# Kernel optimization log

Hardware: AMD Instinct MI355X
Metric: run time of the kernel (lower is better)

## Reference

```python
import jax, jax.numpy as jnp
import numpy as np
import math

NO, NR, E = 100000, 1000, 1000000
DO, DR, DE, H, OM = 64, 32, 4, 64, 32


def setup_inputs() -> dict:
    key = jax.random.key(0)
    ks = jax.random.split(key, 20)
    s = lambda k, sh: jax.random.normal(k, sh, dtype=jnp.float32) * 0.05
    inp = {
        'x_order': jax.random.normal(ks[0], (NO, DO), dtype=jnp.float32),
        'x_rider': jax.random.normal(ks[1], (NR, DR), dtype=jnp.float32),
        'edge_attr': jax.random.normal(ks[2], (E, DE), dtype=jnp.float32),
        'order_idx': jax.random.randint(ks[3], (E,), 0, NO),
        'rider_idx': jax.random.randint(ks[4], (E,), 0, NR),
        'omega_encoded': jax.random.normal(ks[5], (OM,), dtype=jnp.float32),
        # TransformerConv params (heads=1)
        'Wk': s(ks[6], (DO, H)), 'bk': jnp.zeros((H,), jnp.float32),
        'Wq': s(ks[7], (DR, H)), 'bq': jnp.zeros((H,), jnp.float32),
        'Wv': s(ks[8], (DO, H)), 'bv': jnp.zeros((H,), jnp.float32),
        'We': s(ks[9], (DE, H)),  # lin_edge, bias=False in PyG
        'Wskip': s(ks[10], (DR, H)), 'bskip': jnp.zeros((H,), jnp.float32),
        # order_proj
        'Wp': s(ks[11], (DO, H)), 'bp': jnp.zeros((H,), jnp.float32),
        # residual MLP: Linear(2H+OM,128) -> ReLU -> Linear(128,1)
        'W1': s(ks[12], (2 * H + OM, 128)), 'b1': jnp.zeros((128,), jnp.float32),
        'W2': s(ks[13], (128, 1)), 'b2': jnp.zeros((1,), jnp.float32),
    }
    return inp


def _segment_softmax(alpha, seg, num_segments):
    m = jax.ops.segment_max(alpha, seg, num_segments=num_segments)
    m = jnp.where(jnp.isfinite(m), m, 0.0)
    ex = jnp.exp(alpha - m[seg])
    denom = jax.ops.segment_sum(ex, seg, num_segments=num_segments)
    return ex / (denom[seg] + 1e-16)


def reference(x_order, x_rider, edge_attr, order_idx, rider_idx, omega_encoded,
              Wk, bk, Wq, bq, Wv, bv, We, Wskip, bskip, Wp, bp, W1, b1, W2, b2):
    scale = 1.0 / math.sqrt(H)
    # TransformerConv((order, rider) -> rider), heads=1, edge_dim
    q = x_rider @ Wq + bq            # [NR, H]
    k = x_order @ Wk + bk            # [NO, H]
    v = x_order @ Wv + bv            # [NO, H]
    e = edge_attr @ We               # [E, H]
    k_j = k[order_idx] + e           # [E, H]
    v_j = v[order_idx] + e           # [E, H]
    alpha = jnp.sum(q[rider_idx] * k_j, axis=-1) * scale  # [E]
    alpha = _segment_softmax(alpha, rider_idx, NR)
    agg = jax.ops.segment_sum(alpha[:, None] * v_j, rider_idx, num_segments=NR)  # [NR, H]
    rider_emb = agg + x_rider @ Wskip + bskip  # root/skip connection

    # edge scoring
    order_proj = x_order @ Wp + bp   # [NO, H]
    oe = order_proj[order_idx]       # [E, H]
    re = rider_emb[rider_idx]        # [E, H]
    dot = jnp.sum(oe * re, axis=-1) * scale  # [E]
    omega_expand = jnp.broadcast_to(omega_encoded[None, :], (oe.shape[0], OM))
    resid_in = jnp.concatenate([oe, re, omega_expand], axis=-1)  # [E, 2H+OM]
    hmid = jax.nn.relu(resid_in @ W1 + b1)
    resid = (hmid @ W2 + b2)[:, 0]
    return jnp.clip(dot + resid, -10.0, 10.0)
```

## Files before the change

### kernel.cpp

```cpp
#include <hip/hip_runtime.h>
#include <hip/hip_bf16.h>
#include <math.h>
#include <stdint.h>

#define NO_N 100000
#define NR_N 1000
#define E_N  1000000
#define SB     250
#define SCHUNK 4000
#define KVP_TILES 1563
#define KVP_BLKS 1024
#define MAXTILES 17008

typedef short bf16x8 __attribute__((ext_vector_type(8)));
typedef float floatx4 __attribute__((ext_vector_type(4)));

__device__ __forceinline__ unsigned short bfu(float x) {
    union { __hip_bfloat16 h; unsigned short u; } c;
    c.h = __float2bfloat16(x);
    return c.u;
}
__device__ __forceinline__ float bflo(unsigned int u) {
    return __uint_as_float(u << 16);
}
__device__ __forceinline__ float bfhi(unsigned int u) {
    return __uint_as_float(u & 0xffff0000u);
}

__global__ __launch_bounds__(256) void k_front(
    const float* __restrict__ xr,
    const float* __restrict__ Wq, const float* __restrict__ bq,
    const float* __restrict__ Wskip, const float* __restrict__ bskip,
    const float* __restrict__ We,
    float* __restrict__ q, float* __restrict__ skip, float* __restrict__ t,
    const float* __restrict__ W1, const float* __restrict__ b1,
    const float* __restrict__ omega, float* __restrict__ b1eff,
    unsigned short* __restrict__ w1t,
    const float* __restrict__ x,
    const float* __restrict__ Wk, const float* __restrict__ bk,
    const float* __restrict__ Wv, const float* __restrict__ bv,
    const float* __restrict__ Wp, const float* __restrict__ bp,
    unsigned short* __restrict__ kb, unsigned short* __restrict__ vb,
    unsigned short* __restrict__ pb,
    const int* __restrict__ ridx, int* __restrict__ ghist)
{
    __shared__ __align__(16) char smem[9216];
    const int tid = threadIdx.x;
    const int b = blockIdx.x;

    if (b < 250) {
        float* sx = (float*)smem;
        float* sq = sx + 128;
        int rbase = b * 4;
        if (tid < 128) {
            int rl = tid >> 5, d = tid & 31;
            sx[rl * 32 + d] = xr[(rbase + rl) * 32 + d];
        }
        __syncthreads();
        int rl = tid >> 6, h = tid & 63;
        int r = rbase + rl;
        float aq = bq[h], as = bskip[h];
        #pragma unroll 4
        for (int d = 0; d < 32; ++d) {
            float xv = sx[rl * 32 + d];
            aq += xv * Wq[d * 64 + h];
            as += xv * Wskip[d * 64 + h];
        }
        sq[rl * 64 + h] = aq;
        q[r * 64 + h] = aq;
        skip[r * 64 + h] = as;
        __syncthreads();
        if (tid < 16) {
            int rl2 = tid >> 2, d = tid & 3;
            float acc = 0.f;
            for (int hh = 0; hh < 64; ++hh)
                acc += We[d * 64 + hh] * sq[rl2 * 64 + hh];
            t[(rbase + rl2) * 4 + d] = acc;
        }
    } else if (b == 250) {
        if (tid < 128) {
            float acc = b1[tid];
            #pragma unroll 4
            for (int j = 0; j < 32; ++j)
                acc += omega[j] * W1[(128 + j) * 128 + tid];
            b1eff[tid] = acc;
        }
        for (int idx = tid; idx < 64 * 128; idx += 256) {
            int n = idx >> 6, k = idx & 63;
            w1t[idx] = bfu(W1[k * 128 + n]);
        }
    } else if (b < 251 + KVP_BLKS) {
        unsigned short* sX = (unsigned short*)smem;
        const int wave = tid >> 6, lane = tid & 63;
        const int l15 = lane & 15, quad = lane >> 4;

        bf16x8 bfr[3][2];
        float bias[3];
        unsigned short* outT[3];
        int colc[3];
        #pragma unroll
        for (int ct = 0; ct < 3; ++ct) {
            int n = wave * 48 + ct * 16 + l15;
            int table = n >> 6, c = n & 63;
            const float* W  = (table == 0) ? Wk : (table == 1) ? Wv : Wp;
            const float* bb = (table == 0) ? bk : (table == 1) ? bv : bp;
            bias[ct] = bb[c];
            colc[ct] = c;
            outT[ct] = (table == 0) ? kb : (table == 1) ? vb : pb;
            #pragma unroll
            for (int kf = 0; kf < 2; ++kf) {
                bf16x8 f;
                #pragma unroll
                for (int j = 0; j < 8; ++j)
                    f[j] = (short)bfu(W[(size_t)(kf * 32 + quad * 8 + j) * 64 + c]);
                bfr[ct][kf] = f;
            }
        }

        const int srl = tid >> 2;
        const int sqt = (tid & 3) * 16;

        for (int tile = b - 251; tile < KVP_TILES; tile += KVP_BLKS) {
            int rowbase = tile * 64;
            {
                int row = rowbase + srl;
                unsigned short* dst = sX + srl * 72 + sqt;
                if (row < NO_N) {
                    const float4* src = (const float4*)(x + (size_t)row * 64 + sqt);
                    #pragma unroll
                    for (int i = 0; i < 4; ++i) {
                        float4 a = src[i];
                        ushort4 u = { bfu(a.x), bfu(a.y), bfu(a.z), bfu(a.w) };
                        *(ushort4*)(dst + i * 4) = u;
                    }
                } else {
                    ushort4 z = {0, 0, 0, 0};
                    #pragma unroll
                    for (int i = 0; i < 4; ++i) *(ushort4*)(dst + i * 4) = z;
                }
            }
            __syncthreads();

            floatx4 acc[4][3];
            #pragma unroll
            for (int rt = 0; rt < 4; ++rt)
                #pragma unroll
                for (int ct = 0; ct < 3; ++ct)
                    acc[rt][ct] = (floatx4){bias[ct], bias[ct], bias[ct], bias[ct]};

            #pragma unroll
            for (int rt = 0; rt < 4; ++rt) {
                const unsigned short* ar = sX + (size_t)(rt * 16 + l15) * 72 + quad * 8;
                bf16x8 a0 = *(const bf16x8*)(ar);
                bf16x8 a1 = *(const bf16x8*)(ar + 32);
                #pragma unroll
                for (int ct = 0; ct < 3; ++ct) {
                    floatx4 c = acc[rt][ct];
                    c = __builtin_amdgcn_mfma_f32_16x16x32_bf16(a0, bfr[ct][0], c, 0, 0, 0);
                    c = __builtin_amdgcn_mfma_f32_16x16x32_bf16(a1, bfr[ct][1], c, 0, 0, 0);
                    acc[rt][ct] = c;
                }
            }

            #pragma unroll
            for (int rt = 0; rt < 4; ++rt) {
                int rb = rowbase + rt * 16 + quad * 4;
                #pragma unroll
                for (int ct = 0; ct < 3; ++ct) {
                    unsigned short* o = outT[ct];
                    size_t cbase = colc[ct];
                    #pragma unroll
                    for (int g = 0; g < 4; ++g) {
                        int row = rb + g;
                        if (row < NO_N)
                            o[(size_t)row * 64 + cbase] = bfu(acc[rt][ct][g]);
                    }
                }
            }
            __syncthreads();
        }
    } else {
        int* hc = (int*)smem;
        int hb = b - (251 + KVP_BLKS);
        for (int i = tid; i < NR_N; i += 256) hc[i] = 0;
        __syncthreads();
        int s = hb * SCHUNK;
        for (int i = s + tid; i < s + SCHUNK; i += 256)
            atomicAdd(&hc[ridx[i]], 1);
        __syncthreads();
        for (int i = tid; i < NR_N; i += 256)
            ghist[i * SB + hb] = hc[i];
    }
}

__global__ __launch_bounds__(256) void k_colscan(const int* __restrict__ ghist,
                                                 int* __restrict__ gpre,
                                                 int* __restrict__ counts)
{
    __shared__ int s[256];
    int tid = threadIdx.x, r = blockIdx.x;
    int v = (tid < SB) ? ghist[r * SB + tid] : 0;
    s[tid] = v;
    __syncthreads();
    for (int off = 1; off < 256; off <<= 1) {
        int tv = (tid >= off) ? s[tid - off] : 0;
        __syncthreads();
        s[tid] += tv;
        __syncthreads();
    }
    if (tid < SB) gpre[r * SB + tid] = s[tid] - v;
    if (tid == 255) counts[r] = s[255];
}

__global__ __launch_bounds__(1024) void k_scan(const int* __restrict__ counts,
                                               int* __restrict__ offsets,
                                               int* __restrict__ tilestart)
{
    __shared__ int s[1024];
    int tid = threadIdx.x;
    int c = (tid < NR_N) ? counts[tid] : 0;
    s[tid] = c;
    __syncthreads();
    for (int off = 1; off < 1024; off <<= 1) {
        int tv = (tid >= off) ? s[tid - off] : 0;
        __syncthreads();
        s[tid] += tv;
        __syncthreads();
    }
    if (tid < NR_N) offsets[tid] = s[tid] - c;
    if (tid == NR_N - 1) offsets[NR_N] = s[tid];
    __syncthreads();
    int tc = (tid < NR_N) ? ((c + 63) >> 6) : 0;
    s[tid] = tc;
    __syncthreads();
    for (int off = 1; off < 1024; off <<= 1) {
        int tv = (tid >= off) ? s[tid - off] : 0;
        __syncthreads();
        s[tid] += tv;
        __syncthreads();
    }
    if (tid < NR_N) tilestart[tid] = s[tid] - tc;
    if (tid == NR_N - 1) tilestart[NR_N] = s[tid];
}

__global__ __launch_bounds__(256) void k_trec(const int* __restrict__ tilestart,
                                              const int* __restrict__ offsets,
                                              int4* __restrict__ trec)
{
    int nt = tilestart[NR_N];
    int t = blockIdx.x * 256 + threadIdx.x;
    if (t >= nt) return;
    int lo = 0, hi = NR_N - 1;
    while (lo < hi) {
        int mid = (lo + hi + 1) >> 1;
        if (tilestart[mid] <= t) lo = mid; else hi = mid - 1;
    }
    trec[t] = make_int4(lo, offsets[lo] + ((t - tilestart[lo]) << 6),
                        offsets[lo + 1], 0);
}

__global__ __launch_bounds__(1024) void k_scatter2(
    const int* __restrict__ ridx, const int* __restrict__ oidx,
    const float* __restrict__ ea, const float* __restrict__ t,
    const int* __restrict__ offsets, const int* __restrict__ gpre,
    const int* __restrict__ ghist,
    int4* __restrict__ spack, int* __restrict__ so, int* __restrict__ rank)
{
    __shared__ int stmp[1024];
    __shared__ int lpre[NR_N];
    __shared__ int lcur[NR_N];
    __shared__ int gbase[NR_N];
    __shared__ __align__(16) int4 sbuf[SCHUNK];
    __shared__ int spos[SCHUNK];

    const int tid = threadIdx.x, b = blockIdx.x;

    int v = (tid < NR_N) ? ghist[tid * SB + b] : 0;
    stmp[tid] = v;
    __syncthreads();
    for (int off = 1; off < 1024; off <<= 1) {
        int tv = (tid >= off) ? stmp[tid - off] : 0;
        __syncthreads();
        stmp[tid] += tv;
        __syncthreads();
    }
    if (tid < NR_N) {
        lpre[tid] = stmp[tid] - v;
        lcur[tid] = 0;
        gbase[tid] = offsets[tid] + gpre[tid * SB + b];
    }
    __syncthreads();

    int s = b * SCHUNK;
    for (int i = s + tid; i < s + SCHUNK; i += 1024) {
        int r = ridx[i];
        int o = oidx[i];
        float4 e4 = *(const float4*)(ea + (size_t)i * 4);
        float4 t4 = *(const float4*)(t + r * 4);
        float h = e4.x * t4.x + e4.y * t4.y + e4.z * t4.z + e4.w * t4.w;
        int old = atomicAdd(&lcur[r], 1);
        int lpos = lpre[r] + old;
        int gp = gbase[r] + old;
        int4 pk;
        pk.x = o;
        pk.y = __float_as_int(h);
        pk.z = (int)((unsigned)bfu(e4.x) | ((unsigned)bfu(e4.y) << 16));
        pk.w = (int)((unsigned)bfu(e4.z) | ((unsigned)bfu(e4.w) << 16));
        sbuf[lpos] = pk;
        spos[lpos] = gp;
        rank[i] = gp;
    }
    __syncthreads();

    for (int l = tid; l < SCHUNK; l += 1024) {
        int4 pk = sbuf[l];
        int gp = spos[l];
        spack[gp] = pk;
        so[gp] = pk.x;
    }
}

__global__ __launch_bounds__(512) void k_rider(
    const int* __restrict__ offsets, const int4* __restrict__ spack,
    const float* __restrict__ q,
    const unsigned short* __restrict__ kb, const unsigned short* __restrict__ vb,
    const float* __restrict__ We, const float* __restrict__ skip,
    const float* __restrict__ W1, const float* __restrict__ b1eff,
    unsigned short* __restrict__ embb, float* __restrict__ Br)
{
    __shared__ float sQ[64];
    __shared__ int2 sOX[8][64];
    __shared__ float rv[8][64];
    __shared__ float re4[8][4];
    __shared__ float rd[8];

    int r = blockIdx.x;
    int wave = threadIdx.x >> 6, lane = threadIdx.x & 63;
    if (threadIdx.x < 64) sQ[threadIdx.x] = q[r * 64 + threadIdx.x];
    __syncthreads();

    int beg = offsets[r], end = offsets[r + 1];
    int cnt = end - beg;
    int chunk = (cnt + 7) >> 3;
    int s0 = beg + wave * chunk;
    int s1 = min(s0 + chunk, end);

    float av0 = 0.f, av1 = 0.f, av2 = 0.f, av3 = 0.f;
    float dsum = 0.f;
    float ag0 = 0.f, ag1 = 0.f, ag2 = 0.f, ag3 = 0.f;
    const float2* sQ2 = (const float2*)sQ;

    for (int jb = s0; jb < s1; jb += 64) {
        int j = jb + lane;
        bool valid = (j < s1);
        int4 pk = make_int4(0, 0, 0, 0);
        if (valid) pk = spack[j];
        int oo = pk.x;
        float h = __int_as_float(pk.y);

        const uint4* krow = (const uint4*)(kb + (size_t)oo * 64);
        uint4 K0 = krow[0], K1 = krow[1], K2 = krow[2], K3 = krow[3];
        uint4 K4 = krow[4], K5 = krow[5], K6 = krow[6], K7 = krow[7];
        float a0 = h, a1 = 0.f, a2 = 0.f, a3 = 0.f;
        #define DOT8(Kv, base, A) { \
            float2 qa = sQ2[(base) + 0]; \
            A = fmaf(bflo(Kv.x), qa.x, A); A = fmaf(bfhi(Kv.x), qa.y, A); \
            float2 qb = sQ2[(base) + 1]; \
            A = fmaf(bflo(Kv.y), qb.x, A); A = fmaf(bfhi(Kv.y), qb.y, A); \
            float2 qc = sQ2[(base) + 2]; \
            A = fmaf(bflo(Kv.z), qc.x, A); A = fmaf(bfhi(Kv.z), qc.y, A); \
            float2 qd = sQ2[(base) + 3]; \
            A = fmaf(bflo(Kv.w), qd.x, A); A = fmaf(bfhi(Kv.w), qd.y, A); }
        DOT8(K0, 0, a0) DOT8(K1, 4, a1) DOT8(K2, 8, a2) DOT8(K3, 12, a3)
        DOT8(K4, 16, a0) DOT8(K5, 20, a1) DOT8(K6, 24, a2) DOT8(K7, 28, a3)
        #undef DOT8
        float acc = (a0 + a1) + (a2 + a3);

        float exv = valid ? __expf(acc * 0.125f) : 0.f;
        dsum += exv;
        unsigned int ez = (unsigned int)pk.z, ew = (unsigned int)pk.w;
        ag0 = fmaf(exv, bflo(ez), ag0);
        ag1 = fmaf(exv, bfhi(ez), ag1);
        ag2 = fmaf(exv, bflo(ew), ag2);
        ag3 = fmaf(exv, bfhi(ew), ag3);

        sOX[wave][lane] = make_int2(oo, __float_as_int(exv));

        int nn = min(s1 - jb, 64);
        int i = 0;
        for (; i + 8 <= nn; i += 8) {
            int2 x0 = sOX[wave][i + 0], x1 = sOX[wave][i + 1];
            int2 x2 = sOX[wave][i + 2], x3 = sOX[wave][i + 3];
            int2 x4 = sOX[wave][i + 4], x5 = sOX[wave][i + 5];
            int2 x6 = sOX[wave][i + 6], x7 = sOX[wave][i + 7];
            unsigned short u0 = vb[(size_t)x0.x * 64 + lane];
            unsigned short u1 = vb[(size_t)x1.x * 64 + lane];
            unsigned short u2 = vb[(size_t)x2.x * 64 + lane];
            unsigned short u3 = vb[(size_t)x3.x * 64 + lane];
            unsigned short u4 = vb[(size_t)x4.x * 64 + lane];
            unsigned short u5 = vb[(size_t)x5.x * 64 + lane];
            unsigned short u6 = vb[(size_t)x6.x * 64 + lane];
            unsigned short u7 = vb[(size_t)x7.x * 64 + lane];
            av0 = fmaf(__int_as_float(x0.y), __uint_as_float((unsigned int)u0 << 16), av0);
            av1 = fmaf(__int_as_float(x1.y), __uint_as_float((unsigned int)u1 << 16), av1);
            av2 = fmaf(__int_as_float(x2.y), __uint_as_float((unsigned int)u2 << 16), av2);
            av3 = fmaf(__int_as_float(x3.y), __uint_as_float((unsigned int)u3 << 16), av3);
            av0 = fmaf(__int_as_float(x4.y), __uint_as_float((unsigned int)u4 << 16), av0);
            av1 = fmaf(__int_as_float(x5.y), __uint_as_float((unsigned int)u5 << 16), av1);
            av2 = fmaf(__int_as_float(x6.y), __uint_as_float((unsigned int)u6 << 16), av2);
            av3 = fmaf(__int_as_float(x7.y), __uint_as_float((unsigned int)u7 << 16), av3);
        }
        for (; i < nn; ++i) {
            int2 xx = sOX[wave][i];
            unsigned short uu = vb[(size_t)xx.x * 64 + lane];
            av0 = fmaf(__int_as_float(xx.y), __uint_as_float((unsigned int)uu << 16), av0);
        }
    }

    float aggv = (av0 + av1) + (av2 + av3);

    #pragma unroll
    for (int m = 1; m < 64; m <<= 1) {
        dsum += __shfl_xor(dsum, m);
        ag0 += __shfl_xor(ag0, m);
        ag1 += __shfl_xor(ag1, m);
        ag2 += __shfl_xor(ag2, m);
        ag3 += __shfl_xor(ag3, m);
    }

    rv[wave][lane] = aggv;
    if (lane == 0) {
        rd[wave] = dsum;
        re4[wave][0] = ag0; re4[wave][1] = ag1;
        re4[wave][2] = ag2; re4[wave][3] = ag3;
    }
    __syncthreads();
    if (threadIdx.x < 64) {
        int l = threadIdx.x;
        float av = 0.f, ds = 0.f, a0 = 0.f, a1 = 0.f, a2 = 0.f, a3 = 0.f;
        #pragma unroll
        for (int w = 0; w < 8; ++w) {
            av += rv[w][l]; ds += rd[w];
            a0 += re4[w][0]; a1 += re4[w][1]; a2 += re4[w][2]; a3 += re4[w][3];
        }
        float corr = a0 * We[0 * 64 + l] + a1 * We[1 * 64 + l]
                   + a2 * We[2 * 64 + l] + a3 * We[3 * 64 + l];
        float val = (av + corr) / (ds + 1e-16f) + skip[r * 64 + l];
        embb[r * 64 + l] = bfu(val);
        sQ[l] = val;
    }
    __syncthreads();
    if (threadIdx.x < 128) {
        int c = threadIdx.x;
        float a = b1eff[c];
        #pragma unroll 8
        for (int d = 0; d < 64; ++d)
            a = fmaf(sQ[d], W1[(size_t)(64 + d) * 128 + c], a);
        Br[r * 128 + c] = a;
    }
}

__global__ __launch_bounds__(256) void k_edge2(
    const int* __restrict__ so, const int4* __restrict__ trec,
    const int* __restrict__ tilestart,
    const unsigned short* __restrict__ pb, const unsigned short* __restrict__ embb,
    const float* __restrict__ Br, const unsigned short* __restrict__ w1t,
    const float* __restrict__ W2, const float* __restrict__ b2,
    float* __restrict__ tmp)
{
    const int tid = threadIdx.x;
    const int wave = tid >> 6;
    const int lane = tid & 63;
    const int l15 = lane & 15;
    const int quad = lane >> 4;

    bf16x8 bfr[8][2];
    floatx4 w2q[8];
    #pragma unroll
    for (int ctl = 0; ctl < 8; ++ctl) {
        int n = ctl * 16 + l15;
        bfr[ctl][0] = *(const bf16x8*)(w1t + n * 64 + quad * 8);
        bfr[ctl][1] = *(const bf16x8*)(w1t + n * 64 + 32 + quad * 8);
        w2q[ctl] = *(const floatx4*)(W2 + ctl * 16 + quad * 4);
    }
    float b2v = b2[0];
    const int ntiles = tilestart[NR_N];
    const bf16x8 z8 = (bf16x8){0, 0, 0, 0, 0, 0, 0, 0};

    union U4B { uint4 u; bf16x8 b; };

    const int stride = gridDim.x * 4;
    int tile = blockIdx.x * 4 + wave;
    if (tile >= ntiles) return;

    int4 rr = trec[tile];
    int o_rt[4];
    #pragma unroll
    for (int rt = 0; rt < 4; ++rt)
        o_rt[rt] = so[min(rr.y + rt * 16 + l15, rr.z - 1)];

    for (; tile < ntiles; tile += stride) {
        const int r = rr.x, jb = rr.y, jend = rr.z;

        U4B A0[4], A1[4];
        #pragma unroll
        for (int rt = 0; rt < 4; ++rt) {
            const unsigned short* rowp = pb + (size_t)o_rt[rt] * 64 + quad * 8;
            A0[rt].u = *(const uint4*)(rowp);
            A1[rt].u = *(const uint4*)(rowp + 32);
        }

        int4 rrn = trec[min(tile + stride, ntiles - 1)];
        int o_nx[4];
        #pragma unroll
        for (int rt = 0; rt < 4; ++rt)
            o_nx[rt] = so[min(rrn.y + rt * 16 + l15, rrn.z - 1)];

        const unsigned short* eb = embb + r * 64;
        bf16x8 b80 = z8, b81 = z8;
        if (l15 == 0) {
            b80 = *(const bf16x8*)(eb + quad * 8);
            b81 = *(const bf16x8*)(eb + 32 + quad * 8);
        }

        const float* brrow = Br + r * 128;

        #pragma unroll
        for (int rt = 0; rt < 4; ++rt) {
            floatx4 s4 = (floatx4){0.f, 0.f, 0.f, 0.f};
            #pragma unroll
            for (int ctl = 0; ctl < 8; ++ctl) {
                floatx4 c = *(const floatx4*)(brrow + ctl * 16 + quad * 4);
                c = __builtin_amdgcn_mfma_f32_16x16x32_bf16(bfr[ctl][0], A0[rt].b, c, 0, 0, 0);
                c = __builtin_amdgcn_mfma_f32_16x16x32_bf16(bfr[ctl][1], A1[rt].b, c, 0, 0, 0);
                #pragma unroll
                for (int g = 0; g < 4; ++g)
                    s4[g] = fmaf(fmaxf(c[g], 0.f), w2q[ctl][g], s4[g]);
            }
            floatx4 c8 = (floatx4){0.f, 0.f, 0.f, 0.f};
            c8 = __builtin_amdgcn_mfma_f32_16x16x32_bf16(b80, A0[rt].b, c8, 0, 0, 0);
            c8 = __builtin_amdgcn_mfma_f32_16x16x32_bf16(b81, A1[rt].b, c8, 0, 0, 0);

            float s = (s4[0] + s4[1]) + (s4[2] + s4[3]);

            s += __shfl_xor(s, 16);
            s += __shfl_xor(s, 32);

            if (quad == 0) {
                int pos = jb + rt * 16 + l15;
                if (pos < jend) {
                    float v = s + 0.125f * c8[0] + b2v;
                    tmp[pos] = fminf(fmaxf(v, -10.f), 10.f);
                }
            }
        }

        rr = rrn;
        #pragma unroll
        for (int rt = 0; rt < 4; ++rt) o_rt[rt] = o_nx[rt];
    }
}

__global__ __launch_bounds__(256) void k_perm(const int* __restrict__ rank,
                                              const float* __restrict__ tmp,
                                              float* __restrict__ out)
{
    int i = blockIdx.x * 256 + threadIdx.x;
    if (i < E_N) out[i] = tmp[rank[i]];
}

extern "C" void kernel_launch(void* const* d_in, const int* in_sizes, int n_in,
                              void* d_out, int out_size, void* d_ws, size_t ws_size,
                              hipStream_t stream)
{
    const float* x_order   = (const float*)d_in[0];
    const float* x_rider   = (const float*)d_in[1];
    const float* edge_attr = (const float*)d_in[2];
    const int*   order_idx = (const int*)d_in[3];
    const int*   rider_idx = (const int*)d_in[4];
    const float* omega     = (const float*)d_in[5];
    const float* Wk = (const float*)d_in[6];  const float* bk = (const float*)d_in[7];
    const float* Wq = (const float*)d_in[8];  const float* bq = (const float*)d_in[9];
    const float* Wv = (const float*)d_in[10]; const float* bv = (const float*)d_in[11];
    const float* We = (const float*)d_in[12];
    const float* Wskip = (const float*)d_in[13]; const float* bskip = (const float*)d_in[14];
    const float* Wp = (const float*)d_in[15]; const float* bp = (const float*)d_in[16];
    const float* W1 = (const float*)d_in[17]; const float* b1 = (const float*)d_in[18];
    const float* W2 = (const float*)d_in[19]; const float* b2 = (const float*)d_in[20];
    float* out = (float*)d_out;

    unsigned short* ws_kb = (unsigned short*)d_ws;
    unsigned short* ws_vb = ws_kb + (size_t)NO_N * 64;
    unsigned short* ws_pb = ws_vb + (size_t)NO_N * 64;
    int4* ws_spack = (int4*)(ws_pb + (size_t)NO_N * 64);
    float* ws_tmp  = (float*)ws_spack;
    int*  ws_so    = (int*)(ws_spack + E_N);
    int*  ws_rank  = ws_so + E_N;
    float* wsf     = (float*)(ws_rank + E_N);
    float* ws_q    = wsf;
    float* ws_skip = ws_q + NR_N * 64;
    unsigned short* ws_embb = (unsigned short*)(ws_skip + NR_N * 64);
    float* ws_t    = (float*)(ws_embb + NR_N * 64);
    float* ws_b1e  = ws_t + NR_N * 4;
    unsigned short* ws_w1t = (unsigned short*)(ws_b1e + 128);
    float* ws_Br   = (float*)(ws_w1t + 128 * 64);
    int* ws_counts  = (int*)(ws_Br + NR_N * 128);
    int* ws_offsets = ws_counts + NR_N;
    int* ws_tilest  = ws_offsets + NR_N + 8;
    int* ws_ghist   = ws_tilest + NR_N + 8;
    int* ws_gpre    = ws_ghist + NR_N * SB;
    int4* ws_trec   = (int4*)(((uintptr_t)(ws_gpre + NR_N * SB) + 15) & ~(uintptr_t)15);

    k_front<<<251 + KVP_BLKS + SB, 256, 0, stream>>>(
        x_rider, Wq, bq, Wskip, bskip, We, ws_q, ws_skip, ws_t,
        W1, b1, omega, ws_b1e, ws_w1t,
        x_order, Wk, bk, Wv, bv, Wp, bp, ws_kb, ws_vb, ws_pb,
        rider_idx, ws_ghist);
    k_colscan<<<NR_N, 256, 0, stream>>>(ws_ghist, ws_gpre, ws_counts);
    k_scan<<<1, 1024, 0, stream>>>(ws_counts, ws_offsets, ws_tilest);
    k_trec<<<(MAXTILES + 255) / 256, 256, 0, stream>>>(ws_tilest, ws_offsets, ws_trec);
    k_scatter2<<<SB, 1024, 0, stream>>>(rider_idx, order_idx, edge_attr, ws_t,
                                        ws_offsets, ws_gpre, ws_ghist,
                                        ws_spack, ws_so, ws_rank);
    k_rider<<<NR_N, 512, 0, stream>>>(ws_offsets, ws_spack, ws_q,
                                      ws_kb, ws_vb, We, ws_skip,
                                      W1, ws_b1e, ws_embb, ws_Br);
    k_edge2<<<1024, 256, 0, stream>>>(ws_so, ws_trec, ws_tilest,
                                      ws_pb, ws_embb, ws_Br, ws_w1t, W2, b2, ws_tmp);
    k_perm<<<(E_N + 255) / 256, 256, 0, stream>>>(ws_rank, ws_tmp, out);
}
```

Baseline: 273.2 us.

## Fuse rider aggregation and edge scoring into one per-rider kernel

Merges the per-rider attention aggregation kernel and the tiled edge-scoring MFMA kernel into a single kernel with one block per rider. The rider embedding and its W1 contribution now stay in shared memory instead of going through global buffers. This also removes the tile-start scan, the tile-record kernel and the separate sorted order-index array, which cuts launches and global traffic. In exchange, blocks shrink from 512 to 256 threads, the edge phase can no longer balance tiles across a fixed grid, and the software prefetch of next-tile indices is dropped.

```diff
diff --git a/kernel.cpp b/kernel.cpp
--- a/kernel.cpp
+++ b/kernel.cpp
@@ -10,7 +10,6 @@
 #define SCHUNK 4000
 #define KVP_TILES 1563
 #define KVP_BLKS 1024
-#define MAXTILES 17008
 
 typedef short bf16x8 __attribute__((ext_vector_type(8)));
 typedef float floatx4 __attribute__((ext_vector_type(4)));
@@ -213,8 +212,7 @@
 }
 
 __global__ __launch_bounds__(1024) void k_scan(const int* __restrict__ counts,
-                                               int* __restrict__ offsets,
-                                               int* __restrict__ tilestart)
+                                               int* __restrict__ offsets)
 {
     __shared__ int s[1024];
     int tid = threadIdx.x;
@@ -229,34 +227,6 @@
     }
     if (tid < NR_N) offsets[tid] = s[tid] - c;
     if (tid == NR_N - 1) offsets[NR_N] = s[tid];
-    __syncthreads();
-    int tc = (tid < NR_N) ? ((c + 63) >> 6) : 0;
-    s[tid] = tc;
-    __syncthreads();
-    for (int off = 1; off < 1024; off <<= 1) {
-        int tv = (tid >= off) ? s[tid - off] : 0;
-        __syncthreads();
-        s[tid] += tv;
-        __syncthreads();
-    }
-    if (tid < NR_N) tilestart[tid] = s[tid] - tc;
-    if (tid == NR_N - 1) tilestart[NR_N] = s[tid];
-}
-
-__global__ __launch_bounds__(256) void k_trec(const int* __restrict__ tilestart,
-                                              const int* __restrict__ offsets,
-                                              int4* __restrict__ trec)
-{
-    int nt = tilestart[NR_N];
-    int t = blockIdx.x * 256 + threadIdx.x;
-    if (t >= nt) return;
-    int lo = 0, hi = NR_N - 1;
-    while (lo < hi) {
-        int mid = (lo + hi + 1) >> 1;
-        if (tilestart[mid] <= t) lo = mid; else hi = mid - 1;
-    }
-    trec[t] = make_int4(lo, offsets[lo] + ((t - tilestart[lo]) << 6),
-                        offsets[lo + 1], 0);
 }
 
 __global__ __launch_bounds__(1024) void k_scatter2(
@@ -264,7 +234,7 @@
     const float* __restrict__ ea, const float* __restrict__ t,
     const int* __restrict__ offsets, const int* __restrict__ gpre,
     const int* __restrict__ ghist,
-    int4* __restrict__ spack, int* __restrict__ so, int* __restrict__ rank)
+    int4* __restrict__ spack, int* __restrict__ rank)
 {
     __shared__ int stmp[1024];
     __shared__ int lpre[NR_N];
@@ -314,165 +284,158 @@
 
     for (int l = tid; l < SCHUNK; l += 1024) {
         int4 pk = sbuf[l];
-        int gp = spos[l];
-        spack[gp] = pk;
-        so[gp] = pk.x;
-    }
-}
-
-__global__ __launch_bounds__(512) void k_rider(
+        spack[spos[l]] = pk;
+    }
+}
+
+__global__ __launch_bounds__(256) void k_fused(
     const int* __restrict__ offsets, const int4* __restrict__ spack,
     const float* __restrict__ q,
     const unsigned short* __restrict__ kb, const unsigned short* __restrict__ vb,
     const float* __restrict__ We, const float* __restrict__ skip,
     const float* __restrict__ W1, const float* __restrict__ b1eff,
-    unsigned short* __restrict__ embb, float* __restrict__ Br)
+    const unsigned short* __restrict__ pb, const unsigned short* __restrict__ w1t,
+    const float* __restrict__ W2, const float* __restrict__ b2,
+    float* __restrict__ tmp)
 {
     __shared__ float sQ[64];
-    __shared__ int2 sOX[8][64];
-    __shared__ float rv[8][64];
-    __shared__ float re4[8][4];
-    __shared__ float rd[8];
-
-    int r = blockIdx.x;
-    int wave = threadIdx.x >> 6, lane = threadIdx.x & 63;
+    __shared__ int2 sOX[4][64];
+    __shared__ float rv[4][64];
+    __shared__ float re4[4][4];
+    __shared__ float rd[4];
+    __shared__ __align__(16) unsigned short embL[64];
+    __shared__ __align__(16) float BrL[128];
+
+    const int r = blockIdx.x;
+    const int wave = threadIdx.x >> 6, lane = threadIdx.x & 63;
+    const int l15 = lane & 15, quad = lane >> 4;
+
     if (threadIdx.x < 64) sQ[threadIdx.x] = q[r * 64 + threadIdx.x];
     __syncthreads();
 
-    int beg = offsets[r], end = offsets[r + 1];
-    int cnt = end - beg;
-    int chunk = (cnt + 7) >> 3;
-    int s0 = beg + wave * chunk;
-    int s1 = min(s0 + chunk, end);
-
-    float av0 = 0.f, av1 = 0.f, av2 = 0.f, av3 = 0.f;
-    float dsum = 0.f;
-    float ag0 = 0.f, ag1 = 0.f, ag2 = 0.f, ag3 = 0.f;
-    const float2* sQ2 = (const float2*)sQ;
-
-    for (int jb = s0; jb < s1; jb += 64) {
-        int j = jb + lane;
-        bool valid = (j < s1);
-        int4 pk = make_int4(0, 0, 0, 0);
-        if (valid) pk = spack[j];
-        int oo = pk.x;
-        float h = __int_as_float(pk.y);
-
-        const uint4* krow = (const uint4*)(kb + (size_t)oo * 64);
-        uint4 K0 = krow[0], K1 = krow[1], K2 = krow[2], K3 = krow[3];
-        uint4 K4 = krow[4], K5 = krow[5], K6 = krow[6], K7 = krow[7];
-        float a0 = h, a1 = 0.f, a2 = 0.f, a3 = 0.f;
-        #define DOT8(Kv, base, A) { \
-            float2 qa = sQ2[(base) + 0]; \
-            A = fmaf(bflo(Kv.x), qa.x, A); A = fmaf(bfhi(Kv.x), qa.y, A); \
-            float2 qb = sQ2[(base) + 1]; \
-            A = fmaf(bflo(Kv.y), qb.x, A); A = fmaf(bfhi(Kv.y), qb.y, A); \
-            float2 qc = sQ2[(base) + 2]; \
-            A = fmaf(bflo(Kv.z), qc.x, A); A = fmaf(bfhi(Kv.z), qc.y, A); \
-            float2 qd = sQ2[(base) + 3]; \
-            A = fmaf(bflo(Kv.w), qd.x, A); A = fmaf(bfhi(Kv.w), qd.y, A); }
-        DOT8(K0, 0, a0) DOT8(K1, 4, a1) DOT8(K2, 8, a2) DOT8(K3, 12, a3)
-        DOT8(K4, 16, a0) DOT8(K5, 20, a1) DOT8(K6, 24, a2) DOT8(K7, 28, a3)
-        #undef DOT8
-        float acc = (a0 + a1) + (a2 + a3);
-
-        float exv = valid ? __expf(acc * 0.125f) : 0.f;
-        dsum += exv;
-        unsigned int ez = (unsigned int)pk.z, ew = (unsigned int)pk.w;
-        ag0 = fmaf(exv, bflo(ez), ag0);
-        ag1 = fmaf(exv, bfhi(ez), ag1);
-        ag2 = fmaf(exv, bflo(ew), ag2);
-        ag3 = fmaf(exv, bfhi(ew), ag3);
-
-        sOX[wave][lane] = make_int2(oo, __float_as_int(exv));
-
-        int nn = min(s1 - jb, 64);
-        int i = 0;
-        for (; i + 8 <= nn; i += 8) {
-            int2 x0 = sOX[wave][i + 0], x1 = sOX[wave][i + 1];
-            int2 x2 = sOX[wave][i + 2], x3 = sOX[wave][i + 3];
-            int2 x4 = sOX[wave][i + 4], x5 = sOX[wave][i + 5];
-            int2 x6 = sOX[wave][i + 6], x7 = sOX[wave][i + 7];
-            unsigned short u0 = vb[(size_t)x0.x * 64 + lane];
-            unsigned short u1 = vb[(size_t)x1.x * 64 + lane];
-            unsigned short u2 = vb[(size_t)x2.x * 64 + lane];
-            unsigned short u3 = vb[(size_t)x3.x * 64 + lane];
-            unsigned short u4 = vb[(size_t)x4.x * 64 + lane];
-            unsigned short u5 = vb[(size_t)x5.x * 64 + lane];
-            unsigned short u6 = vb[(size_t)x6.x * 64 + lane];
-            unsigned short u7 = vb[(size_t)x7.x * 64 + lane];
-            av0 = fmaf(__int_as_float(x0.y), __uint_as_float((unsigned int)u0 << 16), av0);
-            av1 = fmaf(__int_as_float(x1.y), __uint_as_float((unsigned int)u1 << 16), av1);
-            av2 = fmaf(__int_as_float(x2.y), __uint_as_float((unsigned int)u2 << 16), av2);
-            av3 = fmaf(__int_as_float(x3.y), __uint_as_float((unsigned int)u3 << 16), av3);
-            av0 = fmaf(__int_as_float(x4.y), __uint_as_float((unsigned int)u4 << 16), av0);
-            av1 = fmaf(__int_as_float(x5.y), __uint_as_float((unsigned int)u5 << 16), av1);
-            av2 = fmaf(__int_as_float(x6.y), __uint_as_float((unsigned int)u6 << 16), av2);
-            av3 = fmaf(__int_as_float(x7.y), __uint_as_float((unsigned int)u7 << 16), av3);
-        }
-        for (; i < nn; ++i) {
-            int2 xx = sOX[wave][i];
-            unsigned short uu = vb[(size_t)xx.x * 64 + lane];
-            av0 = fmaf(__int_as_float(xx.y), __uint_as_float((unsigned int)uu << 16), av0);
-        }
-    }
-
-    float aggv = (av0 + av1) + (av2 + av3);
-
-    #pragma unroll
-    for (int m = 1; m < 64; m <<= 1) {
-        dsum += __shfl_xor(dsum, m);
-        ag0 += __shfl_xor(ag0, m);
-        ag1 += __shfl_xor(ag1, m);
-        ag2 += __shfl_xor(ag2, m);
-        ag3 += __shfl_xor(ag3, m);
-    }
-
-    rv[wave][lane] = aggv;
-    if (lane == 0) {
-        rd[wave] = dsum;
-        re4[wave][0] = ag0; re4[wave][1] = ag1;
-        re4[wave][2] = ag2; re4[wave][3] = ag3;
-    }
-    __syncthreads();
-    if (threadIdx.x < 64) {
-        int l = threadIdx.x;
-        float av = 0.f, ds = 0.f, a0 = 0.f, a1 = 0.f, a2 = 0.f, a3 = 0.f;
+    const int beg = offsets[r], end = offsets[r + 1];
+    const int cnt = end - beg;
+
+    {
+        int chunk = (cnt + 3) >> 2;
+        int s0 = beg + wave * chunk;
+        int s1 = min(s0 + chunk, end);
+
+        float av0 = 0.f, av1 = 0.f, av2 = 0.f, av3 = 0.f;
+        float dsum = 0.f;
+        float ag0 = 0.f, ag1 = 0.f, ag2 = 0.f, ag3 = 0.f;
+        const float2* sQ2 = (const float2*)sQ;
+
+        for (int jb = s0; jb < s1; jb += 64) {
+            int j = jb + lane;
+            bool valid = (j < s1);
+            int4 pk = make_int4(0, 0, 0, 0);
+            if (valid) pk = spack[j];
+            int oo = pk.x;
+            float h = __int_as_float(pk.y);
+
+            const uint4* krow = (const uint4*)(kb + (size_t)oo * 64);
+            uint4 K0 = krow[0], K1 = krow[1], K2 = krow[2], K3 = krow[3];
+            uint4 K4 = krow[4], K5 = krow[5], K6 = krow[6], K7 = krow[7];
+            float a0 = h, a1 = 0.f, a2 = 0.f, a3 = 0.f;
+            #define DOT8(Kv, base, A) { \
+                float2 qa = sQ2[(base) + 0]; \
+                A = fmaf(bflo(Kv.x), qa.x, A); A = fmaf(bfhi(Kv.x), qa.y, A); \
+                float2 qb = sQ2[(base) + 1]; \
+                A = fmaf(bflo(Kv.y), qb.x, A); A = fmaf(bfhi(Kv.y), qb.y, A); \
+                float2 qc = sQ2[(base) + 2]; \
+                A = fmaf(bflo(Kv.z), qc.x, A); A = fmaf(bfhi(Kv.z), qc.y, A); \
+                float2 qd = sQ2[(base) + 3]; \
+                A = fmaf(bflo(Kv.w), qd.x, A); A = fmaf(bfhi(Kv.w), qd.y, A); }
+            DOT8(K0, 0, a0) DOT8(K1, 4, a1) DOT8(K2, 8, a2) DOT8(K3, 12, a3)
+            DOT8(K4, 16, a0) DOT8(K5, 20, a1) DOT8(K6, 24, a2) DOT8(K7, 28, a3)
+            #undef DOT8
+            float acc = (a0 + a1) + (a2 + a3);
+
+            float exv = valid ? __expf(acc * 0.125f) : 0.f;
+            dsum += exv;
+            unsigned int ez = (unsigned int)pk.z, ew = (unsigned int)pk.w;
+            ag0 = fmaf(exv, bflo(ez), ag0);
+            ag1 = fmaf(exv, bfhi(ez), ag1);
+            ag2 = fmaf(exv, bflo(ew), ag2);
+            ag3 = fmaf(exv, bfhi(ew), ag3);
+
+            sOX[wave][lane] = make_int2(oo, __float_as_int(exv));
+
+            int nn = min(s1 - jb, 64);
+            int i = 0;
+            for (; i + 8 <= nn; i += 8) {
+                int2 x0 = sOX[wave][i + 0], x1 = sOX[wave][i + 1];
+                int2 x2 = sOX[wave][i + 2], x3 = sOX[wave][i + 3];
+                int2 x4 = sOX[wave][i + 4], x5 = sOX[wave][i + 5];
+                int2 x6 = sOX[wave][i + 6], x7 = sOX[wave][i + 7];
+                unsigned short u0 = vb[(size_t)x0.x * 64 + lane];
+                unsigned short u1 = vb[(size_t)x1.x * 64 + lane];
+                unsigned short u2 = vb[(size_t)x2.x * 64 + lane];
+                unsigned short u3 = vb[(size_t)x3.x * 64 + lane];
+                unsigned short u4 = vb[(size_t)x4.x * 64 + lane];
+                unsigned short u5 = vb[(size_t)x5.x * 64 + lane];
+                unsigned short u6 = vb[(size_t)x6.x * 64 + lane];
+                unsigned short u7 = vb[(size_t)x7.x * 64 + lane];
+                av0 = fmaf(__int_as_float(x0.y), __uint_as_float((unsigned int)u0 << 16), av0);
+                av1 = fmaf(__int_as_float(x1.y), __uint_as_float((unsigned int)u1 << 16), av1);
+                av2 = fmaf(__int_as_float(x2.y), __uint_as_float((unsigned int)u2 << 16), av2);
+                av3 = fmaf(__int_as_float(x3.y), __uint_as_float((unsigned int)u3 << 16), av3);
+                av0 = fmaf(__int_as_float(x4.y), __uint_as_float((unsigned int)u4 << 16), av0);
+                av1 = fmaf(__int_as_float(x5.y), __uint_as_float((unsigned int)u5 << 16), av1);
+                av2 = fmaf(__int_as_float(x6.y), __uint_as_float((unsigned int)u6 << 16), av2);
+                av3 = fmaf(__int_as_float(x7.y), __uint_as_float((unsigned int)u7 << 16), av3);
+            }
+            for (; i < nn; ++i) {
+                int2 xx = sOX[wave][i];
+                unsigned short uu = vb[(size_t)xx.x * 64 + lane];
+                av0 = fmaf(__int_as_float(xx.y), __uint_as_float((unsigned int)uu << 16), av0);
+            }
+        }
+
+        float aggv = (av0 + av1) + (av2 + av3);
+
         #pragma unroll
-        for (int w = 0; w < 8; ++w) {
-            av += rv[w][l]; ds += rd[w];
-            a0 += re4[w][0]; a1 += re4[w][1]; a2 += re4[w][2]; a3 += re4[w][3];
-        }
-        float corr = a0 * We[0 * 64 + l] + a1 * We[1 * 64 + l]
-                   + a2 * We[2 * 64 + l] + a3 * We[3 * 64 + l];
-        float val = (av + corr) / (ds + 1e-16f) + skip[r * 64 + l];
-        embb[r * 64 + l] = bfu(val);
-        sQ[l] = val;
-    }
-    __syncthreads();
-    if (threadIdx.x < 128) {
-        int c = threadIdx.x;
-        float a = b1eff[c];
-        #pragma unroll 8
-        for (int d = 0; d < 64; ++d)
-            a = fmaf(sQ[d], W1[(size_t)(64 + d) * 128 + c], a);
-        Br[r * 128 + c] = a;
-    }
-}
-
-__global__ __launch_bounds__(256) void k_edge2(
-    const int* __restrict__ so, const int4* __restrict__ trec,
-    const int* __restrict__ tilestart,
-    const unsigned short* __restrict__ pb, const unsigned short* __restrict__ embb,
-    const float* __restrict__ Br, const unsigned short* __restrict__ w1t,
-    const float* __restrict__ W2, const float* __restrict__ b2,
-    float* __restrict__ tmp)
-{
-    const int tid = threadIdx.x;
-    const int wave = tid >> 6;
-    const int lane = tid & 63;
-    const int l15 = lane & 15;
-    const int quad = lane >> 4;
+        for (int m = 1; m < 64; m <<= 1) {
+            dsum += __shfl_xor(dsum, m);
+            ag0 += __shfl_xor(ag0, m);
+            ag1 += __shfl_xor(ag1, m);
+            ag2 += __shfl_xor(ag2, m);
+            ag3 += __shfl_xor(ag3, m);
+        }
+
+        rv[wave][lane] = aggv;
+        if (lane == 0) {
+            rd[wave] = dsum;
+            re4[wave][0] = ag0; re4[wave][1] = ag1;
+            re4[wave][2] = ag2; re4[wave][3] = ag3;
+        }
+        __syncthreads();
+        if (threadIdx.x < 64) {
+            int l = threadIdx.x;
+            float av = 0.f, ds = 0.f, a0 = 0.f, a1 = 0.f, a2 = 0.f, a3 = 0.f;
+            #pragma unroll
+            for (int w = 0; w < 4; ++w) {
+                av += rv[w][l]; ds += rd[w];
+                a0 += re4[w][0]; a1 += re4[w][1]; a2 += re4[w][2]; a3 += re4[w][3];
+            }
+            float corr = a0 * We[0 * 64 + l] + a1 * We[1 * 64 + l]
+                       + a2 * We[2 * 64 + l] + a3 * We[3 * 64 + l];
+            float val = (av + corr) / (ds + 1e-16f) + skip[r * 64 + l];
+            embL[l] = bfu(val);
+            sQ[l] = val;
+        }
+        __syncthreads();
+        if (threadIdx.x < 128) {
+            int c = threadIdx.x;
+            float a = b1eff[c];
+            #pragma unroll 8
+            for (int d = 0; d < 64; ++d)
+                a = fmaf(sQ[d], W1[(size_t)(64 + d) * 128 + c], a);
+            BrL[c] = a;
+        }
+        __syncthreads();
+    }
 
     bf16x8 bfr[8][2];
     floatx4 w2q[8];
@@ -484,23 +447,23 @@
         w2q[ctl] = *(const floatx4*)(W2 + ctl * 16 + quad * 4);
     }
     float b2v = b2[0];
-    const int ntiles = tilestart[NR_N];
     const bf16x8 z8 = (bf16x8){0, 0, 0, 0, 0, 0, 0, 0};
+    bf16x8 b80 = z8, b81 = z8;
+    if (l15 == 0) {
+        b80 = *(const bf16x8*)(embL + quad * 8);
+        b81 = *(const bf16x8*)(embL + 32 + quad * 8);
+    }
 
     union U4B { uint4 u; bf16x8 b; };
-
-    const int stride = gridDim.x * 4;
-    int tile = blockIdx.x * 4 + wave;
-    if (tile >= ntiles) return;
-
-    int4 rr = trec[tile];
-    int o_rt[4];
-    #pragma unroll
-    for (int rt = 0; rt < 4; ++rt)
-        o_rt[rt] = so[min(rr.y + rt * 16 + l15, rr.z - 1)];
-
-    for (; tile < ntiles; tile += stride) {
-        const int r = rr.x, jb = rr.y, jend = rr.z;
+    const int ntile = (cnt + 63) >> 6;
+
+    for (int t = wave; t < ntile; t += 4) {
+        int jb = beg + t * 64;
+
+        int o_rt[4];
+        #pragma unroll
+        for (int rt = 0; rt < 4; ++rt)
+            o_rt[rt] = spack[min(jb + rt * 16 + l15, end - 1)].x;
 
         U4B A0[4], A1[4];
         #pragma unroll
@@ -510,54 +473,33 @@
             A1[rt].u = *(const uint4*)(rowp + 32);
         }
 
-        int4 rrn = trec[min(tile + stride, ntiles - 1)];
-        int o_nx[4];
-        #pragma unroll
-        for (int rt = 0; rt < 4; ++rt)
-            o_nx[rt] = so[min(rrn.y + rt * 16 + l15, rrn.z - 1)];
-
-        const unsigned short* eb = embb + r * 64;
-        bf16x8 b80 = z8, b81 = z8;
-        if (l15 == 0) {
-            b80 = *(const bf16x8*)(eb + quad * 8);
-            b81 = *(const bf16x8*)(eb + 32 + quad * 8);
-        }
-
-        const float* brrow = Br + r * 128;
-
         #pragma unroll
         for (int rt = 0; rt < 4; ++rt) {
-            floatx4 s4 = (floatx4){0.f, 0.f, 0.f, 0.f};
+            float s = 0.f;
             #pragma unroll
             for (int ctl = 0; ctl < 8; ++ctl) {
-                floatx4 c = *(const floatx4*)(brrow + ctl * 16 + quad * 4);
+                floatx4 c = *(const floatx4*)(BrL + ctl * 16 + quad * 4);
                 c = __builtin_amdgcn_mfma_f32_16x16x32_bf16(bfr[ctl][0], A0[rt].b, c, 0, 0, 0);
                 c = __builtin_amdgcn_mfma_f32_16x16x32_bf16(bfr[ctl][1], A1[rt].b, c, 0, 0, 0);
                 #pragma unroll
                 for (int g = 0; g < 4; ++g)
-                    s4[g] = fmaf(fmaxf(c[g], 0.f), w2q[ctl][g], s4[g]);
+                    s = fmaf(fmaxf(c[g], 0.f), w2q[ctl][g], s);
             }
             floatx4 c8 = (floatx4){0.f, 0.f, 0.f, 0.f};
             c8 = __builtin_amdgcn_mfma_f32_16x16x32_bf16(b80, A0[rt].b, c8, 0, 0, 0);
             c8 = __builtin_amdgcn_mfma_f32_16x16x32_bf16(b81, A1[rt].b, c8, 0, 0, 0);
 
-            float s = (s4[0] + s4[1]) + (s4[2] + s4[3]);
-
             s += __shfl_xor(s, 16);
             s += __shfl_xor(s, 32);
 
             if (quad == 0) {
                 int pos = jb + rt * 16 + l15;
-                if (pos < jend) {
+                if (pos < end) {
                     float v = s + 0.125f * c8[0] + b2v;
                     tmp[pos] = fminf(fmaxf(v, -10.f), 10.f);
                 }
             }
         }
-
-        rr = rrn;
-        #pragma unroll
-        for (int rt = 0; rt < 4; ++rt) o_rt[rt] = o_nx[rt];
     }
 }
 
@@ -593,23 +535,18 @@
     unsigned short* ws_vb = ws_kb + (size_t)NO_N * 64;
     unsigned short* ws_pb = ws_vb + (size_t)NO_N * 64;
     int4* ws_spack = (int4*)(ws_pb + (size_t)NO_N * 64);
-    float* ws_tmp  = (float*)ws_spack;
-    int*  ws_so    = (int*)(ws_spack + E_N);
-    int*  ws_rank  = ws_so + E_N;
+    float* ws_tmp  = (float*)(ws_spack + E_N);
+    int*  ws_rank  = (int*)(ws_tmp + E_N);
     float* wsf     = (float*)(ws_rank + E_N);
     float* ws_q    = wsf;
     float* ws_skip = ws_q + NR_N * 64;
-    unsigned short* ws_embb = (unsigned short*)(ws_skip + NR_N * 64);
-    float* ws_t    = (float*)(ws_embb + NR_N * 64);
+    float* ws_t    = ws_skip + NR_N * 64;
     float* ws_b1e  = ws_t + NR_N * 4;
     unsigned short* ws_w1t = (unsigned short*)(ws_b1e + 128);
-    float* ws_Br   = (float*)(ws_w1t + 128 * 64);
-    int* ws_counts  = (int*)(ws_Br + NR_N * 128);
+    int* ws_counts  = (int*)(ws_w1t + 128 * 64);
     int* ws_offsets = ws_counts + NR_N;
-    int* ws_tilest  = ws_offsets + NR_N + 8;
-    int* ws_ghist   = ws_tilest + NR_N + 8;
+    int* ws_ghist   = ws_offsets + NR_N + 8;
     int* ws_gpre    = ws_ghist + NR_N * SB;
-    int4* ws_trec   = (int4*)(((uintptr_t)(ws_gpre + NR_N * SB) + 15) & ~(uintptr_t)15);
 
     k_front<<<251 + KVP_BLKS + SB, 256, 0, stream>>>(
         x_rider, Wq, bq, Wskip, bskip, We, ws_q, ws_skip, ws_t,
@@ -617,15 +554,12 @@
         x_order, Wk, bk, Wv, bv, Wp, bp, ws_kb, ws_vb, ws_pb,
         rider_idx, ws_ghist);
     k_colscan<<<NR_N, 256, 0, stream>>>(ws_ghist, ws_gpre, ws_counts);
-    k_scan<<<1, 1024, 0, stream>>>(ws_counts, ws_offsets, ws_tilest);
-    k_trec<<<(MAXTILES + 255) / 256, 256, 0, stream>>>(ws_tilest, ws_offsets, ws_trec);
+    k_scan<<<1, 1024, 0, stream>>>(ws_counts, ws_offsets);
     k_scatter2<<<SB, 1024, 0, stream>>>(rider_idx, order_idx, edge_attr, ws_t,
                                         ws_offsets, ws_gpre, ws_ghist,
-                                        ws_spack, ws_so, ws_rank);
-    k_rider<<<NR_N, 512, 0, stream>>>(ws_offsets, ws_spack, ws_q,
+                                        ws_spack, ws_rank);
+    k_fused<<<NR_N, 256, 0, stream>>>(ws_offsets, ws_spack, ws_q,
                                       ws_kb, ws_vb, We, ws_skip,
-                                      W1, ws_b1e, ws_embb, ws_Br);
-    k_edge2<<<1024, 256, 0, stream>>>(ws_so, ws_trec, ws_tilest,
-                                      ws_pb, ws_embb, ws_Br, ws_w1t, W2, b2, ws_tmp);
+                                      W1, ws_b1e, ws_pb, ws_w1t, W2, b2, ws_tmp);
     k_perm<<<(E_N + 255) / 256, 256, 0, stream>>>(ws_rank, ws_tmp, out);
 }
```

Result: no change. 268.7 us (median of 3 runs) (-1.6%).
